# Kernel optimization log

Hardware: AMD Instinct MI355X
Metric: run time of the kernel (lower is better)

Reference implementation:

```python
import jax, jax.numpy as jnp
import numpy as np

B, S, H = 4, 1024, 4096
NH, NKV, HD = 32, 8, 128
LEVEL = 256


def lsq_quant(x, s, sym):
    # LSQ fake quantization with grad-scale on s and STE round.
    if sym:
        qn, qp = -LEVEL // 2, LEVEL // 2 - 1
    else:
        qn, qp = 0, LEVEL - 1
    g = 1.0 / np.sqrt(x.size * qp)
    s_sc = s * g + jax.lax.stop_gradient(s - s * g)  # value == s, grad scaled by g
    xs = jnp.clip(x / s_sc, qn, qp)
    xq = xs + jax.lax.stop_gradient(jnp.round(xs) - xs)  # STE round
    return xq * s_sc


def rotate_half(x):
    d = x.shape[-1] // 2
    return jnp.concatenate([-x[..., d:], x[..., :d]], axis=-1)


def setup_inputs() -> dict:
    key = jax.random.key(0)
    ks = jax.random.split(key, 8)
    hidden_states = jax.random.normal(ks[0], (B, S, H), dtype=jnp.float32)
    # real RoPE tables (theta=10000)
    inv_freq = 1.0 / (10000.0 ** (np.arange(0, HD, 2, dtype=np.float32) / HD))
    pos = np.arange(S, dtype=np.float32)
    freqs = np.outer(pos, inv_freq)                      # [S, HD/2]
    emb = np.concatenate([freqs, freqs], axis=-1)        # [S, HD]
    cos = jnp.broadcast_to(jnp.cos(emb)[None], (B, S, HD)).astype(jnp.float32)
    sin = jnp.broadcast_to(jnp.sin(emb)[None], (B, S, HD)).astype(jnp.float32)
    # additive causal mask [B,1,S,S]
    neg = jnp.finfo(jnp.float32).min
    causal = jnp.where(jnp.tril(jnp.ones((S, S), bool)), 0.0, neg)
    attention_mask = jnp.broadcast_to(causal[None, None], (B, 1, S, S)).astype(jnp.float32)
    std = 1.0 / np.sqrt(H)
    Wq = jax.random.normal(ks[1], (NH * HD, H), dtype=jnp.float32) * std
    Wk = jax.random.normal(ks[2], (NKV * HD, H), dtype=jnp.float32) * std
    Wv = jax.random.normal(ks[3], (NKV * HD, H), dtype=jnp.float32) * std
    Wo = jax.random.normal(ks[4], (H, NH * HD), dtype=jnp.float32) * std
    return {
        "hidden_states": hidden_states, "cos": cos, "sin": sin,
        "attention_mask": attention_mask,
        "Wq": Wq, "Wk": Wk, "Wv": Wv, "Wo": Wo,
        "s_q": jnp.float32(0.05), "s_k": jnp.float32(0.05), "s_v": jnp.float32(0.05),
        "s_attn": jnp.float32(0.05), "s_after": jnp.float32(0.05), "s_o": jnp.float32(0.05),
    }


def reference(hidden_states, cos, sin, attention_mask, Wq, Wk, Wv, Wo,
              s_q, s_k, s_v, s_attn, s_after, s_o):
    b, s, _ = hidden_states.shape
    scaling = HD ** -0.5
    n_rep = NH // NKV
    # projections (torch Linear: x @ W^T), reshape to [B, heads, S, HD]
    q = (hidden_states @ Wq.T).reshape(b, s, NH, HD).transpose(0, 2, 1, 3)
    k = (hidden_states @ Wk.T).reshape(b, s, NKV, HD).transpose(0, 2, 1, 3)
    v = (hidden_states @ Wv.T).reshape(b, s, NKV, HD).transpose(0, 2, 1, 3)
    q = lsq_quant(q, s_q, sym=True)
    k = lsq_quant(k, s_k, sym=True)
    v = lsq_quant(v, s_v, sym=True)
    # rotary embeddings (cos/sin: [B,S,HD] -> broadcast over head dim)
    c = cos[:, None, :, :]
    sn = sin[:, None, :, :]
    q = q * c + rotate_half(q) * sn
    k = k * c + rotate_half(k) * sn
    # repeat KV heads for GQA
    k = jnp.repeat(k, n_rep, axis=1)
    v = jnp.repeat(v, n_rep, axis=1)
    attn = jnp.einsum('bhqd,bhkd->bhqk', q, k) * scaling
    attn = lsq_quant(attn, s_attn, sym=False)
    attn = attn + attention_mask
    attn = jax.nn.softmax(attn.astype(jnp.float32), axis=-1)
    out = jnp.einsum('bhqk,bhkd->bhqd', attn, v)
    out = lsq_quant(out, s_after, sym=False)
    out = out.transpose(0, 2, 1, 3).reshape(b, s, NH * HD)
    out = out @ Wo.T
    out = lsq_quant(out, s_o, sym=True)
    return out, attn
```

## Files before the change

### kernel.cpp

```cpp
#include <hip/hip_runtime.h>
#include <math.h>

#define B_   4
#define S_   1024
#define H_   4096
#define NH_  32
#define NKV_ 8
#define HD_  128
#define M_   (B_*S_)
#define SCALING 0.08838834764831845f

#define R16M 16777216

typedef _Float16 f16;
typedef __attribute__((ext_vector_type(4))) _Float16 f16x4;
typedef __attribute__((ext_vector_type(8))) _Float16 f16x8;
typedef __attribute__((ext_vector_type(4))) float f32x4;

__device__ __forceinline__ float lsq_sym(float x, float s) {
  float xs = x / s;
  xs = fminf(fmaxf(xs, -128.0f), 127.0f);
  return rintf(xs) * s;
}
__device__ __forceinline__ float lsq_asym(float x, float s) {
  float xs = x / s;
  xs = fminf(fmaxf(xs, 0.0f), 255.0f);
  return rintf(xs) * s;
}

struct f16pair { f16 hi, lo; };
__device__ __forceinline__ f16pair cvt_hilo(float x) {
  f16pair r;
  r.hi = (f16)x;
  r.lo = (f16)(x - (float)r.hi);
  return r;
}

__device__ __forceinline__ void gload16(const void* g, void* l) {
  __builtin_amdgcn_global_load_lds((const __attribute__((address_space(1))) void*)g,
                                   (__attribute__((address_space(3))) void*)l, 16, 0, 0);
}

__global__ __launch_bounds__(256)
void split_flat(const float* __restrict__ src, f16* __restrict__ hi, f16* __restrict__ lo)
{
  const size_t i = ((size_t)blockIdx.x * 256 + threadIdx.x) * 4;
  float4 v = *(const float4*)(src + i);
  f16x4 h, l; f16pair p;
  p = cvt_hilo(v.x); h.x = p.hi; l.x = p.lo;
  p = cvt_hilo(v.y); h.y = p.hi; l.y = p.lo;
  p = cvt_hilo(v.z); h.z = p.hi; l.z = p.lo;
  p = cvt_hilo(v.w); h.w = p.hi; l.w = p.lo;
  *(f16x4*)(hi + i) = h;
  *(f16x4*)(lo + i) = l;
}

__global__ __launch_bounds__(256)
void split_wqk(const float* __restrict__ W, f16* __restrict__ hi, f16* __restrict__ lo)
{
  const size_t i = ((size_t)blockIdx.x * 256 + threadIdx.x) * 4;
  const int n = (int)(i >> 12);
  const int k = (int)(i & 4095);
  const int d = n & 127;
  const int prow = (n & ~127) | ((d < 64) ? (d << 1) : (((d - 64) << 1) | 1));
  float4 v = *(const float4*)(W + i);
  f16x4 h, l; f16pair p;
  p = cvt_hilo(v.x); h.x = p.hi; l.x = p.lo;
  p = cvt_hilo(v.y); h.y = p.hi; l.y = p.lo;
  p = cvt_hilo(v.z); h.z = p.hi; l.z = p.lo;
  p = cvt_hilo(v.w); h.w = p.hi; l.w = p.lo;
  *(f16x4*)(hi + (size_t)prow * 4096 + k) = h;
  *(f16x4*)(lo + (size_t)prow * 4096 + k) = l;
}

template<int ATERMS, int EPI>
__global__ __launch_bounds__(256, 2)
void gemm_mfma(const f16* __restrict__ Ahi, const f16* __restrict__ Alo, int lda,
               const f16* __restrict__ Bhi, const f16* __restrict__ Blo, int ldb,
               float* __restrict__ C, int ldc, int K,
               const float* __restrict__ sA, const float* __restrict__ sQ,
               const float* __restrict__ cosp, const float* __restrict__ sinp,
               f16* __restrict__ o1, f16* __restrict__ o2)
{
  __shared__ f16 sAh[256 * 32];
  __shared__ f16 sAl[(ATERMS == 2) ? 256 * 32 : 64];
  __shared__ f16 sBh[128 * 32];
  __shared__ f16 sBl[128 * 32];

  const int m0 = blockIdx.y << 8;
  const int n0 = blockIdx.x << 7;
  const int t    = threadIdx.x;
  const int lane = t & 63;
  const int wv   = t >> 6;
  const int wm   = (wv >> 1) << 7;
  const int wn   = (wv & 1) << 6;
  const int lrow = lane & 15;
  const int kg   = (lane >> 4) << 3;
  const int fsw  = (lrow & 3) << 3;

  const int sr   = lane >> 2;
  const int slot = lane & 3;
  const int kcs  = ((slot ^ (sr & 3)) << 3);

  f32x4 acc[8][4];
  #pragma unroll
  for (int i = 0; i < 8; ++i)
    #pragma unroll
    for (int j = 0; j < 4; ++j) acc[i][j] = (f32x4){0.f, 0.f, 0.f, 0.f};

  for (int k0 = 0; k0 < K; k0 += 32) {
    #pragma unroll
    for (int i = 0; i < 4; ++i) {
      const int rowb = (wv << 6) + (i << 4);
      const size_t goff = (size_t)(m0 + rowb + sr) * lda + k0 + kcs;
      gload16(Ahi + goff, &sAh[rowb * 32]);
      if constexpr (ATERMS == 2) gload16(Alo + goff, &sAl[rowb * 32]);
    }
    #pragma unroll
    for (int i = 0; i < 2; ++i) {
      const int rowb = (wv << 5) + (i << 4);
      const size_t goff = (size_t)(n0 + rowb + sr) * ldb + k0 + kcs;
      gload16(Bhi + goff, &sBh[rowb * 32]);
      gload16(Blo + goff, &sBl[rowb * 32]);
    }
    __syncthreads();

    f16x8 a[8], bh[4], bl[4];
    #pragma unroll
    for (int j = 0; j < 4; ++j) {
      const int r = wn + (j << 4) + lrow;
      bh[j] = *(const f16x8*)&sBh[r * 32 + (kg ^ fsw)];
      bl[j] = *(const f16x8*)&sBl[r * 32 + (kg ^ fsw)];
    }
    #pragma unroll
    for (int i = 0; i < 8; ++i)
      a[i] = *(const f16x8*)&sAh[(wm + (i << 4) + lrow) * 32 + (kg ^ fsw)];
    #pragma unroll
    for (int i = 0; i < 8; ++i)
      #pragma unroll
      for (int j = 0; j < 4; ++j) {
        acc[i][j] = __builtin_amdgcn_mfma_f32_16x16x32_f16(a[i], bh[j], acc[i][j], 0, 0, 0);
        acc[i][j] = __builtin_amdgcn_mfma_f32_16x16x32_f16(a[i], bl[j], acc[i][j], 0, 0, 0);
      }
    if constexpr (ATERMS == 2) {
      #pragma unroll
      for (int i = 0; i < 8; ++i)
        a[i] = *(const f16x8*)&sAl[(wm + (i << 4) + lrow) * 32 + (kg ^ fsw)];
      #pragma unroll
      for (int i = 0; i < 8; ++i)
        #pragma unroll
        for (int j = 0; j < 4; ++j)
          acc[i][j] = __builtin_amdgcn_mfma_f32_16x16x32_f16(a[i], bh[j], acc[i][j], 0, 0, 0);
    }
    __syncthreads();
  }

  const float s = *sA;
  float sQv = 1.0f;
  if constexpr (EPI == 1) sQv = *sQ;

  #pragma unroll
  for (int i = 0; i < 8; ++i)
    #pragma unroll
    for (int j = 0; j < 4; ++j) {
      const int gc = n0 + wn + (j << 4) + lrow;
      #pragma unroll
      for (int r = 0; r < 4; ++r) {
        const int gr = m0 + wm + (i << 4) + ((lane >> 4) << 2) + r;
        float x = acc[i][j][r];
        if constexpr (EPI == 1) {
          C[(size_t)gr * ldc + gc] = lsq_sym(x * s, sQv);
        } else if constexpr (EPI == 2 || EPI == 4) {
          float qv = lsq_sym(x, s);
          float pv = __shfl_xor(qv, 1);
          const int dperm = gc & 127;
          const int dpair = dperm >> 1;
          float cs = cosp[(size_t)gr * HD_ + dpair];
          float sn = sinp[(size_t)gr * HD_ + dpair];
          float ro = (gc & 1) ? (qv * cs + pv * sn) : (qv * cs - pv * sn);
          f16pair hp = cvt_hilo(ro);
          if constexpr (EPI == 2) {
            o1[(size_t)gr * 4096 + gc] = hp.hi;
            o2[(size_t)gr * 4096 + gc] = hp.lo;
          } else {
            const int bb = gr >> 10, ki = gr & 1023;
            const int kvh = gc >> 7;
            const int c = dperm >> 5, sub = (dperm >> 3) & 3, e = dperm & 7;
            const size_t base = ((size_t)(bb * 8 + kvh) << 18) + ((size_t)(ki >> 4) << 12)
                              + (c << 10) + ((ki & 15) << 3) + (sub << 7) + e;
            o1[base] = hp.hi;
            o1[base + 512] = hp.lo;
          }
        } else {
          float xi = rintf(fminf(fmaxf(x / s, -128.0f), 127.0f));
          const int bb = gr >> 10, ss = gr & 1023;
          const int kv = gc >> 7,  dd = gc & 127;
          o1[(((size_t)(bb * 8 + kv) * 128 + dd) << 10) + ss] = (f16)xi;
        }
      }
    }
}

__global__ __launch_bounds__(256)
void attn_fused(const f16* __restrict__ qhiB, const f16* __restrict__ qloB,
                const f16* __restrict__ kfrag, float* __restrict__ attn,
                const float* __restrict__ saP)
{
  const int b = blockIdx.z, h = blockIdx.y, qi0 = blockIdx.x << 4;
  const int t = threadIdx.x, lane = t & 63, w = t >> 6;
  const int lc = lane & 15, lg = lane >> 4;
  const int kvh = h >> 2;
  const float sa = *saP;

  f16x8 qh[4], ql[4];
  {
    const size_t qoff = (size_t)(b * S_ + qi0 + lc) * 4096 + h * HD_;
    #pragma unroll
    for (int c = 0; c < 4; ++c) {
      const int off = c * 32 + lg * 8;
      qh[c] = *(const f16x8*)(qhiB + qoff + off);
      ql[c] = *(const f16x8*)(qloB + qoff + off);
    }
  }

  f32x4 acc[16];
  #pragma unroll
  for (int tt = 0; tt < 16; ++tt) acc[tt] = (f32x4){0.f, 0.f, 0.f, 0.f};

  const int qimax = qi0 + 15;
  const f16* kb = kfrag + ((size_t)(b * 8 + kvh) << 18);

  #pragma unroll
  for (int tt = 0; tt < 16; ++tt) {
    const int ki0 = (w << 8) + (tt << 4);
    if (ki0 <= qimax) {
      const f16* kt = kb + ((size_t)((w << 4) + tt) << 12) + lane * 8;
      #pragma unroll
      for (int c = 0; c < 4; ++c) {
        f16x8 kh = *(const f16x8*)(kt + (c << 10));
        f16x8 kl = *(const f16x8*)(kt + (c << 10) + 512);
        acc[tt] = __builtin_amdgcn_mfma_f32_16x16x32_f16(kh, qh[c], acc[tt], 0, 0, 0);
        acc[tt] = __builtin_amdgcn_mfma_f32_16x16x32_f16(kh, ql[c], acc[tt], 0, 0, 0);
        acc[tt] = __builtin_amdgcn_mfma_f32_16x16x32_f16(kl, qh[c], acc[tt], 0, 0, 0);
      }
    }
  }

  const int qi = qi0 + lc;

  float m = -3.0e38f;
  #pragma unroll
  for (int tt = 0; tt < 16; ++tt) {
    const int kib = (w << 8) + (tt << 4) + (lg << 2);
    #pragma unroll
    for (int r = 0; r < 4; ++r) {
      float x = (kib + r <= qi) ? lsq_asym(acc[tt][r] * SCALING, sa) : -3.0e38f;
      acc[tt][r] = x;
      m = fmaxf(m, x);
    }
  }
  m = fmaxf(m, __shfl_xor(m, 16));
  m = fmaxf(m, __shfl_xor(m, 32));

  __shared__ float redM[4][16];
  __shared__ float redS[4][16];
  if (lg == 0) redM[w][lc] = m;
  __syncthreads();
  float mrow = fmaxf(fmaxf(redM[0][lc], redM[1][lc]), fmaxf(redM[2][lc], redM[3][lc]));

  float ssum = 0.f;
  #pragma unroll
  for (int tt = 0; tt < 16; ++tt) {
    #pragma unroll
    for (int r = 0; r < 4; ++r) {
      float p = __expf(acc[tt][r] - mrow);
      acc[tt][r] = p;
      ssum += p;
    }
  }
  ssum += __shfl_xor(ssum, 16);
  ssum += __shfl_xor(ssum, 32);
  if (lg == 0) redS[w][lc] = ssum;
  __syncthreads();
  const float inv = 1.0f / (redS[0][lc] + redS[1][lc] + redS[2][lc] + redS[3][lc]);

  float* orow = attn + ((size_t)(b * NH_ + h) * S_ + qi) * S_ + (w << 8) + (lg << 2);
  #pragma unroll
  for (int tt = 0; tt < 16; ++tt) {
    float4 v;
    v.x = acc[tt][0] * inv;
    v.y = acc[tt][1] * inv;
    v.z = acc[tt][2] * inv;
    v.w = acc[tt][3] * inv;
    *(float4*)(orow + (tt << 4)) = v;
  }
}

__global__ __launch_bounds__(256)
void pv_mfma(const float* __restrict__ attn, const f16* __restrict__ vt,
             f16* __restrict__ pvint,
             const float* __restrict__ svP, const float* __restrict__ safP)
{
  const int b = blockIdx.z, h = blockIdx.y, q0 = blockIdx.x << 7;
  const int t = threadIdx.x, lane = t & 63, w = t >> 6;
  const int wd = (w >> 1) << 6, wq = (w & 1) << 6;
  const int lc = lane & 15, lg = lane >> 4;
  const int kvh = h >> 2;
  const float sv = *svP, saf = *safP;

  f32x4 acc[4][4];
  #pragma unroll
  for (int i = 0; i < 4; ++i)
    #pragma unroll
    for (int j = 0; j < 4; ++j) acc[i][j] = (f32x4){0.f, 0.f, 0.f, 0.f};

  const float* Pbase = attn + (size_t)(b * NH_ + h) * S_ * S_;
  const int kimax = q0 + 128;

  for (int ki0 = 0; ki0 < kimax; ki0 += 32) {
    f16x8 a[4];
    #pragma unroll
    for (int i = 0; i < 4; ++i) {
      const int d = wd + i * 16 + lc;
      a[i] = *(const f16x8*)(vt + (((size_t)(b * 8 + kvh) * 128 + d) << 10) + ki0 + lg * 8);
    }
    #pragma unroll
    for (int j = 0; j < 4; ++j) {
      const int q = q0 + wq + j * 16 + lc;
      const float* pp = Pbase + (size_t)q * S_ + ki0 + lg * 8;
      float4 p0 = *(const float4*)pp;
      float4 p1 = *(const float4*)(pp + 4);
      f16x8 bh, bl; f16pair pr;
      pr = cvt_hilo(p0.x); bh[0] = pr.hi; bl[0] = pr.lo;
      pr = cvt_hilo(p0.y); bh[1] = pr.hi; bl[1] = pr.lo;
      pr = cvt_hilo(p0.z); bh[2] = pr.hi; bl[2] = pr.lo;
      pr = cvt_hilo(p0.w); bh[3] = pr.hi; bl[3] = pr.lo;
      pr = cvt_hilo(p1.x); bh[4] = pr.hi; bl[4] = pr.lo;
      pr = cvt_hilo(p1.y); bh[5] = pr.hi; bl[5] = pr.lo;
      pr = cvt_hilo(p1.z); bh[6] = pr.hi; bl[6] = pr.lo;
      pr = cvt_hilo(p1.w); bh[7] = pr.hi; bl[7] = pr.lo;
      #pragma unroll
      for (int i = 0; i < 4; ++i) {
        acc[i][j] = __builtin_amdgcn_mfma_f32_16x16x32_f16(a[i], bh, acc[i][j], 0, 0, 0);
        acc[i][j] = __builtin_amdgcn_mfma_f32_16x16x32_f16(a[i], bl, acc[i][j], 0, 0, 0);
      }
    }
  }

  #pragma unroll
  for (int i = 0; i < 4; ++i)
    #pragma unroll
    for (int j = 0; j < 4; ++j) {
      const int q  = q0 + wq + j * 16 + lc;
      const int d0 = wd + i * 16 + lg * 4;
      f16x4 v;
      #pragma unroll
      for (int r = 0; r < 4; ++r) {
        float x = sv * acc[i][j][r];
        x = fminf(fmaxf(x / saf, 0.0f), 255.0f);
        v[r] = (f16)rintf(x);
      }
      *(f16x4*)(pvint + (size_t)(b * S_ + q) * 4096 + h * HD_ + d0) = v;
    }
}

extern "C" void kernel_launch(void* const* d_in, const int* in_sizes, int n_in,
                              void* d_out, int out_size, void* d_ws, size_t ws_size,
                              hipStream_t stream)
{
  const float* hidden = (const float*)d_in[0];
  const float* cosp   = (const float*)d_in[1];
  const float* sinp   = (const float*)d_in[2];
  const float* Wq     = (const float*)d_in[4];
  const float* Wk     = (const float*)d_in[5];
  const float* Wv     = (const float*)d_in[6];
  const float* Wo     = (const float*)d_in[7];
  const float* s_q    = (const float*)d_in[8];
  const float* s_k    = (const float*)d_in[9];
  const float* s_v    = (const float*)d_in[10];
  const float* s_attn = (const float*)d_in[11];
  const float* s_after= (const float*)d_in[12];
  const float* s_o    = (const float*)d_in[13];

  float* out  = (float*)d_out;
  float* attn = out + (size_t)M_ * H_;

  f16* wsf   = (f16*)d_ws;
  f16* Qhi   = wsf;
  f16* Qlo   = wsf + (size_t)R16M;
  f16* Kfrag = wsf + (size_t)2*R16M;
  f16* Vt    = wsf + (size_t)2*R16M + (size_t)R16M/2;
  f16* PVint = wsf;
  f16* WoHi  = wsf + (size_t)R16M;
  f16* WoLo  = wsf + (size_t)2*R16M;

  f16* scr = (f16*)attn;
  f16* hHi = scr;
  f16* hLo = scr + (size_t)R16M;
  f16* wHi = scr + (size_t)2*R16M;
  f16* wLo = scr + (size_t)3*R16M;

  dim3 blk(256, 1, 1);

  split_flat<<<dim3(16384), blk, 0, stream>>>(hidden, hHi, hLo);
  split_wqk<<<dim3(16384), blk, 0, stream>>>(Wq, wHi, wLo);
  gemm_mfma<2,2><<<dim3(32,16), blk, 0, stream>>>(hHi, hLo, H_, wHi, wLo, H_,
      nullptr, 0, H_, s_q, nullptr, cosp, sinp, Qhi, Qlo);

  split_wqk<<<dim3(4096), blk, 0, stream>>>(Wk, wHi, wLo);
  gemm_mfma<2,4><<<dim3(8,16), blk, 0, stream>>>(hHi, hLo, H_, wHi, wLo, H_,
      nullptr, 0, H_, s_k, nullptr, cosp, sinp, Kfrag, nullptr);

  split_flat<<<dim3(4096), blk, 0, stream>>>(Wv, wHi, wLo);
  gemm_mfma<2,3><<<dim3(8,16), blk, 0, stream>>>(hHi, hLo, H_, wHi, wLo, H_,
      nullptr, 0, H_, s_v, nullptr, nullptr, nullptr, Vt, nullptr);

  attn_fused<<<dim3(64, NH_, B_), blk, 0, stream>>>(Qhi, Qlo, Kfrag, attn, s_attn);

  pv_mfma<<<dim3(8, NH_, B_), blk, 0, stream>>>(attn, Vt, PVint, s_v, s_after);

  split_flat<<<dim3(16384), blk, 0, stream>>>(Wo, WoHi, WoLo);
  gemm_mfma<1,1><<<dim3(32,16), blk, 0, stream>>>(PVint, nullptr, 4096,
      WoHi, WoLo, 4096, out, H_, H_, s_after, s_o, nullptr, nullptr, nullptr, nullptr);
}
```

Measured before the change: 1.761 ms.

## Fuse Q, K, V projections into one concatenated-weight GEMM launch

Splits Wq, Wk and Wv into one concatenated hi/lo weight buffer and runs a single 48x16-block GEMM instead of three separate launches. The epilogue picks the Q, K or V path per block from its column offset. This removes two launches and fills the GPU better than the small 8x16 K and V grids, which each left many CUs idle. In exchange the concatenated weights need more scratch space, and the epilogue now branches on a runtime region value.

```diff
diff --git a/kernel.cpp b/kernel.cpp
--- a/kernel.cpp
+++ b/kernel.cpp
@@ -78,9 +78,11 @@
 void gemm_mfma(const f16* __restrict__ Ahi, const f16* __restrict__ Alo, int lda,
                const f16* __restrict__ Bhi, const f16* __restrict__ Blo, int ldb,
                float* __restrict__ C, int ldc, int K,
-               const float* __restrict__ sA, const float* __restrict__ sQ,
+               const float* __restrict__ sQp, const float* __restrict__ sKp,
+               const float* __restrict__ sVp,
                const float* __restrict__ cosp, const float* __restrict__ sinp,
-               f16* __restrict__ o1, f16* __restrict__ o2)
+               f16* __restrict__ qhi, f16* __restrict__ qlo,
+               f16* __restrict__ kfrag, f16* __restrict__ vt)
 {
   __shared__ f16 sAh[256 * 32];
   __shared__ f16 sAl[(ATERMS == 2) ? 256 * 32 : 64];
@@ -155,9 +157,14 @@
     __syncthreads();
   }
 
-  const float s = *sA;
-  float sQv = 1.0f;
-  if constexpr (EPI == 1) sQv = *sQ;
+  int region = 0;
+  float s, sQv = 1.0f;
+  if constexpr (EPI == 1) {
+    s = *sQp; sQv = *sKp;
+  } else {
+    region = (n0 < 4096) ? 0 : ((n0 < 5120) ? 1 : 2);
+    s = (region == 0) ? *sQp : (region == 1) ? *sKp : *sVp;
+  }
 
   #pragma unroll
   for (int i = 0; i < 8; ++i)
@@ -170,32 +177,36 @@
         float x = acc[i][j][r];
         if constexpr (EPI == 1) {
           C[(size_t)gr * ldc + gc] = lsq_sym(x * s, sQv);
-        } else if constexpr (EPI == 2 || EPI == 4) {
-          float qv = lsq_sym(x, s);
-          float pv = __shfl_xor(qv, 1);
-          const int dperm = gc & 127;
-          const int dpair = dperm >> 1;
-          float cs = cosp[(size_t)gr * HD_ + dpair];
-          float sn = sinp[(size_t)gr * HD_ + dpair];
-          float ro = (gc & 1) ? (qv * cs + pv * sn) : (qv * cs - pv * sn);
-          f16pair hp = cvt_hilo(ro);
-          if constexpr (EPI == 2) {
-            o1[(size_t)gr * 4096 + gc] = hp.hi;
-            o2[(size_t)gr * 4096 + gc] = hp.lo;
+        } else {
+          if (region <= 1) {
+            float qv = lsq_sym(x, s);
+            float pv = __shfl_xor(qv, 1);
+            const int dperm = gc & 127;
+            const int dpair = dperm >> 1;
+            float cs = cosp[(size_t)gr * HD_ + dpair];
+            float sn = sinp[(size_t)gr * HD_ + dpair];
+            float ro = (gc & 1) ? (qv * cs + pv * sn) : (qv * cs - pv * sn);
+            f16pair hp = cvt_hilo(ro);
+            if (region == 0) {
+              qhi[(size_t)gr * 4096 + gc] = hp.hi;
+              qlo[(size_t)gr * 4096 + gc] = hp.lo;
+            } else {
+              const int lcol = gc - 4096;
+              const int bb = gr >> 10, ki = gr & 1023;
+              const int kvh = lcol >> 7;
+              const int c = dperm >> 5, sub = (dperm >> 3) & 3, e = dperm & 7;
+              const size_t base = ((size_t)(bb * 8 + kvh) << 18) + ((size_t)(ki >> 4) << 12)
+                                + (c << 10) + ((ki & 15) << 3) + (sub << 7) + e;
+              kfrag[base] = hp.hi;
+              kfrag[base + 512] = hp.lo;
+            }
           } else {
-            const int bb = gr >> 10, ki = gr & 1023;
-            const int kvh = gc >> 7;
-            const int c = dperm >> 5, sub = (dperm >> 3) & 3, e = dperm & 7;
-            const size_t base = ((size_t)(bb * 8 + kvh) << 18) + ((size_t)(ki >> 4) << 12)
-                              + (c << 10) + ((ki & 15) << 3) + (sub << 7) + e;
-            o1[base] = hp.hi;
-            o1[base + 512] = hp.lo;
+            float xi = rintf(fminf(fmaxf(x / s, -128.0f), 127.0f));
+            const int lcol = gc - 5120;
+            const int bb = gr >> 10, ss = gr & 1023;
+            const int kv = lcol >> 7, dd = lcol & 127;
+            vt[(((size_t)(bb * 8 + kv) * 128 + dd) << 10) + ss] = (f16)xi;
           }
-        } else {
-          float xi = rintf(fminf(fmaxf(x / s, -128.0f), 127.0f));
-          const int bb = gr >> 10, ss = gr & 1023;
-          const int kv = gc >> 7,  dd = gc & 127;
-          o1[(((size_t)(bb * 8 + kv) * 128 + dd) << 10) + ss] = (f16)xi;
         }
       }
     }
@@ -395,25 +406,20 @@
   f16* WoLo  = wsf + (size_t)2*R16M;
 
   f16* scr = (f16*)attn;
-  f16* hHi = scr;
-  f16* hLo = scr + (size_t)R16M;
-  f16* wHi = scr + (size_t)2*R16M;
-  f16* wLo = scr + (size_t)3*R16M;
+  f16* hHi   = scr;
+  f16* hLo   = scr + (size_t)R16M;
+  f16* WcatH = scr + (size_t)2*R16M;
+  f16* WcatL = scr + (size_t)2*R16M + (size_t)6144*4096;
 
   dim3 blk(256, 1, 1);
 
   split_flat<<<dim3(16384), blk, 0, stream>>>(hidden, hHi, hLo);
-  split_wqk<<<dim3(16384), blk, 0, stream>>>(Wq, wHi, wLo);
-  gemm_mfma<2,2><<<dim3(32,16), blk, 0, stream>>>(hHi, hLo, H_, wHi, wLo, H_,
-      nullptr, 0, H_, s_q, nullptr, cosp, sinp, Qhi, Qlo);
-
-  split_wqk<<<dim3(4096), blk, 0, stream>>>(Wk, wHi, wLo);
-  gemm_mfma<2,4><<<dim3(8,16), blk, 0, stream>>>(hHi, hLo, H_, wHi, wLo, H_,
-      nullptr, 0, H_, s_k, nullptr, cosp, sinp, Kfrag, nullptr);
-
-  split_flat<<<dim3(4096), blk, 0, stream>>>(Wv, wHi, wLo);
-  gemm_mfma<2,3><<<dim3(8,16), blk, 0, stream>>>(hHi, hLo, H_, wHi, wLo, H_,
-      nullptr, 0, H_, s_v, nullptr, nullptr, nullptr, Vt, nullptr);
+  split_wqk <<<dim3(16384), blk, 0, stream>>>(Wq, WcatH, WcatL);
+  split_wqk <<<dim3(4096),  blk, 0, stream>>>(Wk, WcatH + (size_t)4096*4096, WcatL + (size_t)4096*4096);
+  split_flat<<<dim3(4096),  blk, 0, stream>>>(Wv, WcatH + (size_t)5120*4096, WcatL + (size_t)5120*4096);
+
+  gemm_mfma<2,5><<<dim3(48,16), blk, 0, stream>>>(hHi, hLo, H_, WcatH, WcatL, H_,
+      nullptr, 0, H_, s_q, s_k, s_v, cosp, sinp, Qhi, Qlo, Kfrag, Vt);
 
   attn_fused<<<dim3(64, NH_, B_), blk, 0, stream>>>(Qhi, Qlo, Kfrag, attn, s_attn);
 
@@ -421,5 +427,6 @@
 
   split_flat<<<dim3(16384), blk, 0, stream>>>(Wo, WoHi, WoLo);
   gemm_mfma<1,1><<<dim3(32,16), blk, 0, stream>>>(PVint, nullptr, 4096,
-      WoHi, WoLo, 4096, out, H_, H_, s_after, s_o, nullptr, nullptr, nullptr, nullptr);
-}
+      WoHi, WoLo, 4096, out, H_, H_, s_after, s_o, nullptr, nullptr, nullptr,
+      nullptr, nullptr, nullptr, nullptr);
+}
```

After: 1.580 ms. -10.3%, faster.
